# Performance work log

Measured on AMD Instinct MI355X. Metric: run time of the kernel, lower is better.

Reference implementation:

```python
import jax, jax.numpy as jnp
import numpy as np

B, N, K, H, NF = 4, 4096, 20, 64, 128
EPS = 1e-5  # BatchNorm eps (inference mode)


def _knn_idx(x):
    # x: (B, C, N); returns indices of K nearest neighbors (incl. self), (B, N, K)
    xx = jnp.sum(x * x, axis=1)                      # (B, N)
    inner = jnp.einsum('bcn,bcm->bnm', x, x)         # (B, N, N)
    neg_dist = 2.0 * inner - xx[:, :, None] - xx[:, None, :]
    return jax.lax.top_k(neg_dist, K)[1]


def _graph_feat(x, first):
    # x: (B, C, N) -> edge features (B, C', N, K)
    idx = _knn_idx(x)                                # (B, N, K)
    xt = jnp.transpose(x, (0, 2, 1))                 # (B, N, C)
    nb = jax.vmap(lambda f, i: f[i])(xt, idx)        # (B, N, K, C)
    nb = jnp.transpose(nb, (0, 3, 1, 2))             # (B, C, N, K)
    c = jnp.broadcast_to(x[:, :, :, None], nb.shape)
    parts = [nb - c]
    if first:  # cross term only in first block (3-dim coords)
        parts.append(jnp.cross(c, nb, axis=1))
    parts.append(c)
    return jnp.concatenate(parts, axis=1)


def _conv_bn_lrelu(x, W, g, b, m, v):
    # 1x1 conv (no bias) + BatchNorm (inference) + LeakyReLU(0.2)
    y = jnp.einsum('oc,bc...->bo...', W, x)
    scale = g / jnp.sqrt(v + EPS)
    sh = (1, -1) + (1,) * (y.ndim - 2)
    y = y * scale.reshape(sh) + (b - m * scale).reshape(sh)
    return jnp.where(y >= 0, y, 0.2 * y)


def _forward(x, layers, We, Wh, bh):
    x = jnp.transpose(x, (0, 2, 1))                  # (B, 3, N)
    outs = []
    for li in range(4):
        gf = _graph_feat(x, li == 0)                 # (B, cin, N, K)
        y = _conv_bn_lrelu(gf, *layers[li])          # (B, cout, N, K)
        x = jnp.max(y, axis=-1)                      # max-pool over neighbors
        outs.append(x)
    cat = jnp.concatenate(outs, axis=1)              # (B, 512, N)
    y = _conv_bn_lrelu(cat, *layers[4])              # final Conv1d block
    y = jnp.max(y, axis=-1)                          # global max over points
    emb = y @ We.T                                   # Linear(512, NF, bias=False)
    return emb @ Wh.T + bh                           # embedding_head


def setup_inputs() -> dict:
    key = jax.random.key(0)
    ks = jax.random.split(key, 40)

    def nrm(k, shape, s=0.1):
        return jax.random.normal(k, shape, jnp.float32) * s

    inp = {'x': jax.random.normal(ks[0], (B, N, 3), jnp.float32)}
    dims = [(9, H), (2 * H, H), (2 * H, 2 * H), (4 * H, 4 * H), (8 * H, 8 * H)]
    i = 1
    for li, (cin, cout) in enumerate(dims):
        inp['W%d' % li] = nrm(ks[i], (cout, cin)); i += 1
        inp['g%d' % li] = 1.0 + nrm(ks[i], (cout,), 0.05); i += 1
        inp['b%d' % li] = nrm(ks[i], (cout,), 0.05); i += 1
        inp['m%d' % li] = nrm(ks[i], (cout,), 0.05); i += 1
        inp['v%d' % li] = 1.0 + jax.random.uniform(ks[i], (cout,)) * 0.1; i += 1
    inp['We'] = nrm(ks[i], (NF, 8 * H)); i += 1
    inp['Wh'] = nrm(ks[i], (NF, NF)); i += 1
    inp['bh'] = nrm(ks[i], (NF,))
    return inp


def reference(x, W0, g0, b0, m0, v0, W1, g1, b1, m1, v1, W2, g2, b2, m2, v2,
              W3, g3, b3, m3, v3, W4, g4, b4, m4, v4, We, Wh, bh):
    layers = [(W0, g0, b0, m0, v0), (W1, g1, b1, m1, v1), (W2, g2, b2, m2, v2),
              (W3, g3, b3, m3, v3), (W4, g4, b4, m4, v4)]
    return _forward(x, layers, We, Wh, bh)
```

## Files before the change

### kernel.cpp

```cpp
#include <hip/hip_runtime.h>
#include <cfloat>

#define N_PTS 4096
#define NB    4
#define KNN   20
#define EPSB  1e-5f
#define NSL   4

typedef short s8v __attribute__((ext_vector_type(8)));
typedef float f4v __attribute__((ext_vector_type(4)));

__device__ __forceinline__ void bf16split(float x, unsigned short* h, unsigned short* l)
{
    unsigned u = __builtin_bit_cast(unsigned, x);
    unsigned hb = (u + 0x7fffu + ((u >> 16) & 1u)) >> 16;
    float hf = __builtin_bit_cast(float, hb << 16);
    float res = x - hf;
    unsigned u2 = __builtin_bit_cast(unsigned, res);
    unsigned lb = (u2 + 0x7fffu + ((u2 >> 16) & 1u)) >> 16;
    *h = (unsigned short)hb;
    *l = (unsigned short)lb;
}

__device__ __forceinline__ unsigned packkey(float d, int lc)
{
    d = fmaxf(d, 0.f);
    unsigned u = __builtin_bit_cast(unsigned, d);
    return (u & 0xFFFFFF00u) | (unsigned)lc;
}

__device__ __forceinline__ void insert20k(unsigned key, unsigned (&k20)[KNN])
{
#pragma unroll
    for (int j = 0; j < KNN; j++) {
        unsigned old = k20[j];
        unsigned lo = old < key ? old : key;
        key = old < key ? key : old;
        k20[j] = lo;
    }
}

__device__ __forceinline__ void gl2lds16(const void* g, void* l)
{
    __builtin_amdgcn_global_load_lds(
        (const __attribute__((address_space(1))) unsigned int*)g,
        (__attribute__((address_space(3))) unsigned int*)l,
        16, 0, 0);
}

__device__ __forceinline__ int swz(int g)
{
    return g ^ (((g >> 3) ^ (g >> 6)) & 7);
}

__global__ __launch_bounds__(256)
void to_bf16_pm(const float* __restrict__ F, long bsF, int ldF, int C, int KDP,
                unsigned short* __restrict__ Ghi, unsigned short* __restrict__ Glo)
{
    int b = blockIdx.y;
    int n = blockIdx.x * 64 + (threadIdx.x & 63);
    int kq = threadIdx.x >> 6;
    const float* Fr = F + (long)b * bsF + (long)n * ldF;
    for (int k0 = kq * 8; k0 < KDP; k0 += 32) {
        s8v hv, lv;
#pragma unroll
        for (int i = 0; i < 8; i++) {
            int k = k0 + i;
            float x = (k < C) ? Fr[k] : 0.f;
            unsigned short h, l;
            bf16split(x, &h, &l);
            hv[i] = (short)h;
            lv[i] = (short)l;
        }
        long o = ((long)b * N_PTS + n) * KDP + k0;
        *(s8v*)&Ghi[o] = hv;
        *(s8v*)&Glo[o] = lv;
    }
}

__global__ void sqnorm_pm(const float* __restrict__ F, float* __restrict__ xx,
                          int C, int ldF, long bsF)
{
    int b = blockIdx.y;
    int i = blockIdx.x * 256 + threadIdx.x;
    const float* r = F + (long)b * bsF + (long)i * ldF;
    float s = 0.f;
    for (int c = 0; c < C; c++) s = fmaf(r[c], r[c], s);
    xx[(long)b * N_PTS + i] = s;
}

template<int KDP>
__global__ __launch_bounds__(256, 3)
void fused_knn_mfma7(const unsigned short* __restrict__ Ghi,
                     const unsigned short* __restrict__ Glo,
                     const float* __restrict__ xx,
                     float* __restrict__ knnd, int* __restrict__ knni)
{
    constexpr int KS = KDP / 32;
    constexpr int TS = 16 * KDP;
    constexpr int NCH = (TS * 2) / 16;
    __shared__ short cbuf[2][2][TS];
    __shared__ unsigned mk[4][16][4][KNN];

    int tid = threadIdx.x;
    int w = tid >> 6, L = tid & 63;
    int n = L & 15;
    int quad = L >> 4;
    int b = blockIdx.z, slice = blockIdx.y;
    int q0 = blockIdx.x * 64, qw = w * 16;
    const unsigned short* Gh = Ghi + (long)b * N_PTS * KDP;
    const unsigned short* Gl = Glo + (long)b * N_PTS * KDP;
    const float* xxb = xx + (long)b * N_PTS;

    s8v qhi[KS], qlo[KS];
    long qbase = (long)(q0 + qw + n) * KDP + quad * 8;
#pragma unroll
    for (int ks = 0; ks < KS; ks++) {
        qhi[ks] = *(const s8v*)&Gh[qbase + ks * 32];
        qlo[ks] = *(const s8v*)&Gl[qbase + ks * 32];
    }
    float xq = xxb[q0 + qw + n];

    unsigned k20[KNN];
#pragma unroll
    for (int j = 0; j < KNN; j++) k20[j] = 0xFFFFFFFFu;

    int po[KS];
#pragma unroll
    for (int ks = 0; ks < KS; ks++) {
        int gL = n * (KDP / 8) + quad + ks * 4;
        po[ks] = swz(gL) * 8;
    }
    int gsrc = swz(tid);

    int w64 = tid & 192;
    {
        long tb = (long)(slice * 1024) * KDP;
        if (tid < NCH) {
            gl2lds16((const char*)(Gh + tb) + gsrc * 16,
                     (char*)&cbuf[0][0][0] + w64 * 16);
            gl2lds16((const char*)(Gl + tb) + gsrc * 16,
                     (char*)&cbuf[0][1][0] + w64 * 16);
        }
    }
    __syncthreads();

    const float* xcp = xxb + slice * 1024 + quad * 4;

    for (int t = 0; t < 64; t++) {
        int cur = t & 1;
        if (t < 63 && tid < NCH) {
            long tb = (long)(slice * 1024 + (t + 1) * 16) * KDP;
            gl2lds16((const char*)(Gh + tb) + gsrc * 16,
                     (char*)&cbuf[cur ^ 1][0][0] + w64 * 16);
            gl2lds16((const char*)(Gl + tb) + gsrc * 16,
                     (char*)&cbuf[cur ^ 1][1][0] + w64 * 16);
        }

        const short* Ch = &cbuf[cur][0][0];
        const short* Cl = &cbuf[cur][1][0];
        f4v acc = {0.f, 0.f, 0.f, 0.f};
#pragma unroll
        for (int ks = 0; ks < KS; ks++) {
            s8v chi = *(const s8v*)&Ch[po[ks]];
            s8v clo = *(const s8v*)&Cl[po[ks]];
            acc = __builtin_amdgcn_mfma_f32_16x16x32_bf16(chi, qhi[ks], acc, 0, 0, 0);
            acc = __builtin_amdgcn_mfma_f32_16x16x32_bf16(chi, qlo[ks], acc, 0, 0, 0);
            acc = __builtin_amdgcn_mfma_f32_16x16x32_bf16(clo, qhi[ks], acc, 0, 0, 0);
        }
        float4 xc4 = *(const float4*)xcp;
        float xcv[4] = {xc4.x, xc4.y, xc4.z, xc4.w};
#pragma unroll
        for (int r = 0; r < 4; r++) {
            float d = xq + xcv[r] - 2.f * acc[r];
            insert20k(packkey(d, t * 4 + r), k20);
        }
        xcp += 16;
        __syncthreads();
    }

#pragma unroll
    for (int j = 0; j < KNN; j++) mk[w][n][quad][j] = k20[j];
    __syncthreads();
    if (L < 16) {
        int p[4] = {0, 0, 0, 0};
        long o = (((long)b * NSL + slice) * N_PTS + (q0 + qw + L)) * KNN;
#pragma unroll
        for (int j = 0; j < KNN; j++) {
            unsigned bd = 0xFFFFFF00u; int bi = 0x7fffffff; int bq = 0;
#pragma unroll
            for (int qd = 0; qd < 4; qd++) {
                unsigned kk = mk[w][L][qd][p[qd]];
                unsigned db = kk & 0xFFFFFF00u;
                int lc = (int)(kk & 0xFFu);
                int ci = slice * 1024 + (lc >> 2) * 16 + qd * 4 + (lc & 3);
                if (db < bd || (db == bd && ci < bi)) { bd = db; bi = ci; bq = qd; }
            }
            knnd[o + j] = __builtin_bit_cast(float, bd);
            knni[o + j] = bi;
            p[bq]++;
        }
    }
}

__global__ void knn_merge4(const float* __restrict__ knnd, const int* __restrict__ knni,
                           int* __restrict__ idxOut)
{
    int id = blockIdx.x * 256 + threadIdx.x;
    int b = id / N_PTS, i = id % N_PTS;
    const float* dl[NSL]; const int* il[NSL];
#pragma unroll
    for (int qt = 0; qt < NSL; qt++) {
        dl[qt] = knnd + (((long)b * NSL + qt) * N_PTS + i) * KNN;
        il[qt] = knni + (((long)b * NSL + qt) * N_PTS + i) * KNN;
    }
    int p[NSL];
#pragma unroll
    for (int qt = 0; qt < NSL; qt++) p[qt] = 0;
    int* o = idxOut + (long)id * KNN;
#pragma unroll
    for (int j = 0; j < KNN; j++) {
        float best = FLT_MAX; int bi = 0x7fffffff; int bq = 0;
#pragma unroll
        for (int qt = 0; qt < NSL; qt++) {
            float vv = (p[qt] < KNN) ? dl[qt][p[qt]] : FLT_MAX;
            int   ci = (p[qt] < KNN) ? il[qt][p[qt]] : 0x7fffffff;
            if (vv < best || (vv == best && ci < bi)) { best = vv; bi = ci; bq = qt; }
        }
        o[j] = bi;
        p[bq]++;
    }
}

template<int KDP>
__global__ __launch_bounds__(256)
void qp_mfma(const unsigned short* __restrict__ Ghi,
             const unsigned short* __restrict__ Glo,
             const unsigned short* __restrict__ Wqh, const unsigned short* __restrict__ Wql,
             const unsigned short* __restrict__ Wph, const unsigned short* __restrict__ Wpl,
             const float* __restrict__ shf,
             float* __restrict__ qv, float* __restrict__ pv, int cout)
{
    constexpr int KS = KDP / 32;
    int tid = threadIdx.x;
    int w = tid >> 6, L = tid & 63;
    int n = L & 15, quad = L >> 4;
    int b = blockIdx.z;
    int p0 = blockIdx.x * 64 + w * 16;

    s8v ah[KS], al[KS];
    long abase = ((long)b * N_PTS + p0 + n) * KDP + quad * 8;
#pragma unroll
    for (int ks = 0; ks < KS; ks++) {
        ah[ks] = *(const s8v*)&Ghi[abase + ks * 32];
        al[ks] = *(const s8v*)&Glo[abase + ks * 32];
    }

#pragma unroll
    for (int oc4 = 0; oc4 < 4; oc4++) {
        int oc = blockIdx.y * 4 + oc4;
        long wbase = (long)(oc * 16 + n) * KDP + quad * 8;
        f4v aq = {0.f, 0.f, 0.f, 0.f};
        f4v ap = {0.f, 0.f, 0.f, 0.f};
#pragma unroll
        for (int ks = 0; ks < KS; ks++) {
            s8v wh = *(const s8v*)&Wqh[wbase + ks * 32];
            s8v wl = *(const s8v*)&Wql[wbase + ks * 32];
            aq = __builtin_amdgcn_mfma_f32_16x16x32_bf16(ah[ks], wh, aq, 0, 0, 0);
            aq = __builtin_amdgcn_mfma_f32_16x16x32_bf16(ah[ks], wl, aq, 0, 0, 0);
            aq = __builtin_amdgcn_mfma_f32_16x16x32_bf16(al[ks], wh, aq, 0, 0, 0);
            s8v ph = *(const s8v*)&Wph[wbase + ks * 32];
            s8v pl = *(const s8v*)&Wpl[wbase + ks * 32];
            ap = __builtin_amdgcn_mfma_f32_16x16x32_bf16(ah[ks], ph, ap, 0, 0, 0);
            ap = __builtin_amdgcn_mfma_f32_16x16x32_bf16(ah[ks], pl, ap, 0, 0, 0);
            ap = __builtin_amdgcn_mfma_f32_16x16x32_bf16(al[ks], ph, ap, 0, 0, 0);
        }
        float sv = shf[oc * 16 + n];
#pragma unroll
        for (int r = 0; r < 4; r++) {
            long pt = p0 + quad * 4 + r;
            long o = ((long)b * N_PTS + pt) * cout + oc * 16 + n;
            qv[o] = aq[r];
            pv[o] = ap[r] + sv;
        }
    }
}

__global__ __launch_bounds__(256)
void conv4g_mfma(const float* __restrict__ cat,
                 const unsigned short* __restrict__ W4h, const unsigned short* __restrict__ W4l,
                 const float* __restrict__ shf, float* __restrict__ Y)
{
    int tid = threadIdx.x;
    int w = tid >> 6, L = tid & 63;
    int n = L & 15, quad = L >> 4;
    int b = blockIdx.z;
    int p0 = blockIdx.x * 64 + w * 16;
    int ob0 = blockIdx.y * 64;

    const float* cr = cat + ((long)b * N_PTS + p0 + n) * 512 + quad * 8;

    f4v acc[4];
#pragma unroll
    for (int c4 = 0; c4 < 4; c4++) acc[c4] = {0.f, 0.f, 0.f, 0.f};

    for (int ks = 0; ks < 16; ks++) {
        float4 f0 = *(const float4*)&cr[ks * 32];
        float4 f1 = *(const float4*)&cr[ks * 32 + 4];
        float fv[8] = {f0.x, f0.y, f0.z, f0.w, f1.x, f1.y, f1.z, f1.w};
        s8v ah, al;
#pragma unroll
        for (int i = 0; i < 8; i++) {
            unsigned short h, l;
            bf16split(fv[i], &h, &l);
            ah[i] = (short)h;
            al[i] = (short)l;
        }
#pragma unroll
        for (int c4 = 0; c4 < 4; c4++) {
            long wb = (long)(ob0 + c4 * 16 + n) * 512 + quad * 8 + ks * 32;
            s8v wh = *(const s8v*)&W4h[wb];
            s8v wl = *(const s8v*)&W4l[wb];
            acc[c4] = __builtin_amdgcn_mfma_f32_16x16x32_bf16(ah, wh, acc[c4], 0, 0, 0);
            acc[c4] = __builtin_amdgcn_mfma_f32_16x16x32_bf16(ah, wl, acc[c4], 0, 0, 0);
            acc[c4] = __builtin_amdgcn_mfma_f32_16x16x32_bf16(al, wh, acc[c4], 0, 0, 0);
        }
    }
#pragma unroll
    for (int c4 = 0; c4 < 4; c4++) {
        int o = ob0 + c4 * 16 + n;
        float sv = shf[o];
#pragma unroll
        for (int r = 0; r < 4; r++) {
            int pt = p0 + quad * 4 + r;
            float y = acc[c4][r] + sv;
            y = y >= 0.f ? y : 0.2f * y;
            Y[((long)b * 512 + o) * N_PTS + pt] = y;
        }
    }
}

__global__ void fold_edge_bf16(const float* __restrict__ W, const float* __restrict__ g,
                               const float* __restrict__ bb, const float* __restrict__ m,
                               const float* __restrict__ v,
                               unsigned short* __restrict__ Wqh, unsigned short* __restrict__ Wql,
                               unsigned short* __restrict__ Wph, unsigned short* __restrict__ Wpl,
                               float* __restrict__ shift, int C, int cout)
{
    int id = blockIdx.x * 256 + threadIdx.x;
    if (id < C * cout) {
        int o = id / C;
        int c = id % C;
        float sc = g[o] * rsqrtf(v[o] + EPSB);
        float wd = W[(long)o * 2 * C + c];
        float wc = W[(long)o * 2 * C + C + c];
        bf16split(sc * wd, &Wqh[id], &Wql[id]);
        bf16split(sc * (wc - wd), &Wph[id], &Wpl[id]);
    }
    if (id < cout) {
        float sc = g[id] * rsqrtf(v[id] + EPSB);
        shift[id] = bb[id] - m[id] * sc;
    }
}

__global__ void fold_plain_bf16(const float* __restrict__ W, const float* __restrict__ g,
                                const float* __restrict__ bb, const float* __restrict__ m,
                                const float* __restrict__ v,
                                unsigned short* __restrict__ W4h, unsigned short* __restrict__ W4l,
                                float* __restrict__ shift, int C, int cout)
{
    int id = blockIdx.x * 256 + threadIdx.x;
    if (id < C * cout) {
        int o = id / C;
        int c = id % C;
        float sc = g[o] * rsqrtf(v[o] + EPSB);
        bf16split(sc * W[(long)o * C + c], &W4h[id], &W4l[id]);
    }
    if (id < cout) {
        float sc = g[id] * rsqrtf(v[id] + EPSB);
        shift[id] = bb[id] - m[id] * sc;
    }
}

__global__ void gather_max_fused(const float* __restrict__ q, const float* __restrict__ p,
                                 const int* __restrict__ idx, float* __restrict__ cat,
                                 int cout, int c_off,
                                 unsigned short* __restrict__ Ghi,
                                 unsigned short* __restrict__ Glo,
                                 float* __restrict__ xx)
{
    int b = blockIdx.y;
    int i = blockIdx.x * 4 + threadIdx.y;
    int tx = threadIdx.x;
    const int* ip = idx + ((long)b * N_PTS + i) * KNN;
    int js[KNN];
#pragma unroll
    for (int k = 0; k < KNN; k++) js[k] = ip[k];
    const float* qb = q + (long)b * N_PTS * cout;
    const float* pb = p + ((long)b * N_PTS + i) * cout;
    float* ob = cat + ((long)b * N_PTS + i) * 512 + c_off;
    float ssum = 0.f;
    for (int o0 = 0; o0 < cout; o0 += 64) {
        int o = o0 + tx;
        float pv = pb[o];
        float mx = -FLT_MAX;
#pragma unroll
        for (int k = 0; k < KNN; k++) {
            float val = qb[(long)js[k] * cout + o] + pv;
            val = val >= 0.f ? val : 0.2f * val;
            mx = fmaxf(mx, val);
        }
        ob[o] = mx;
        if (Ghi) {
            unsigned short h, l;
            bf16split(mx, &h, &l);
            long go = ((long)b * N_PTS + i) * cout + o;
            Ghi[go] = h;
            Glo[go] = l;
            ssum = fmaf(mx, mx, ssum);
        }
    }
    if (Ghi) {
#pragma unroll
        for (int off = 32; off > 0; off >>= 1) ssum += __shfl_xor(ssum, off);
        if (tx == 0) xx[(long)b * N_PTS + i] = ssum;
    }
}

__global__ void edge0_fused(const float* __restrict__ x, const int* __restrict__ idx,
                            const float* __restrict__ W0, const float* __restrict__ g0,
                            const float* __restrict__ b0, const float* __restrict__ m0,
                            const float* __restrict__ v0, float* __restrict__ cat,
                            unsigned short* __restrict__ Ghi,
                            unsigned short* __restrict__ Glo,
                            float* __restrict__ xx)
{
    int b = blockIdx.y;
    int i = blockIdx.x * 4 + threadIdx.y;
    int o = threadIdx.x;
    const float* xc = x + ((long)b * N_PTS + i) * 3;
    float cx = xc[0], cy = xc[1], cz = xc[2];
    float w[9];
#pragma unroll
    for (int c = 0; c < 9; c++) w[c] = W0[o * 9 + c];
    float sc = g0[o] * rsqrtf(v0[o] + EPSB);
    float sh = b0[o] - m0[o] * sc;
    const int* ip = idx + ((long)b * N_PTS + i) * KNN;
    float mx = -FLT_MAX;
#pragma unroll
    for (int k = 0; k < KNN; k++) {
        const float* xn = x + ((long)b * N_PTS + ip[k]) * 3;
        float nx = xn[0], ny = xn[1], nz = xn[2];
        float dx = nx - cx, dy = ny - cy, dz = nz - cz;
        float crx = cy * nz - cz * ny;
        float cry = cz * nx - cx * nz;
        float crz = cx * ny - cy * nx;
        float y = w[0] * dx + w[1] * dy + w[2] * dz
                + w[3] * crx + w[4] * cry + w[5] * crz
                + w[6] * cx + w[7] * cy + w[8] * cz;
        y = y * sc + sh;
        y = y >= 0.f ? y : 0.2f * y;
        mx = fmaxf(mx, y);
    }
    cat[((long)b * N_PTS + i) * 512 + o] = mx;
    unsigned short h, l;
    bf16split(mx, &h, &l);
    long go = ((long)b * N_PTS + i) * 64 + o;
    Ghi[go] = h;
    Glo[go] = l;
    float ssum = mx * mx;
#pragma unroll
    for (int off = 32; off > 0; off >>= 1) ssum += __shfl_xor(ssum, off);
    if (o == 0) xx[(long)b * N_PTS + i] = ssum;
}

__global__ void rowmax_kernel(const float* __restrict__ Y, float* __restrict__ ymax)
{
    __shared__ float red[256];
    int b = blockIdx.y, o = blockIdx.x, t = threadIdx.x;
    const float* yb = Y + ((long)b * 512 + o) * N_PTS;
    float mx = -FLT_MAX;
#pragma unroll
    for (int s = 0; s < N_PTS / 256; s++) mx = fmaxf(mx, yb[t + 256 * s]);
    red[t] = mx;
    __syncthreads();
    for (int off = 128; off > 0; off >>= 1) {
        if (t < off) red[t] = fmaxf(red[t], red[t + off]);
        __syncthreads();
    }
    if (t == 0) ymax[(long)b * 512 + o] = red[0];
}

__global__ void head_kernel(const float* __restrict__ ymax, const float* __restrict__ We,
                            const float* __restrict__ Wh, const float* __restrict__ bh,
                            float* __restrict__ out)
{
    __shared__ float emb[128];
    __shared__ float yv[512];
    int b = blockIdx.x, t = threadIdx.x;
    for (int s = t; s < 512; s += 128) yv[s] = ymax[(long)b * 512 + s];
    __syncthreads();
    float acc = 0.f;
    for (int c = 0; c < 512; c++) acc = fmaf(yv[c], We[(long)t * 512 + c], acc);
    emb[t] = acc;
    __syncthreads();
    float acc2 = bh[t];
    for (int ff = 0; ff < 128; ff++) acc2 = fmaf(emb[ff], Wh[(long)t * 128 + ff], acc2);
    out[(long)b * 128 + t] = acc2;
}

extern "C" void kernel_launch(void* const* d_in, const int* in_sizes, int n_in,
                              void* d_out, int out_size, void* d_ws, size_t ws_size,
                              hipStream_t stream)
{
    const float* x = (const float*)d_in[0];
    const float *W[5], *g[5], *bb[5], *m[5], *v[5];
    for (int li = 0; li < 5; li++) {
        W[li]  = (const float*)d_in[1 + li * 5 + 0];
        g[li]  = (const float*)d_in[1 + li * 5 + 1];
        bb[li] = (const float*)d_in[1 + li * 5 + 2];
        m[li]  = (const float*)d_in[1 + li * 5 + 3];
        v[li]  = (const float*)d_in[1 + li * 5 + 4];
    }
    const float* We = (const float*)d_in[26];
    const float* Wh = (const float*)d_in[27];
    const float* bh = (const float*)d_in[28];
    float* out = (float*)d_out;

    float* ws   = (float*)d_ws;
    float* cat  = ws;
    float* qbuf = cat + (long)8388608;
    float* pbuf = qbuf + (long)8388608;
    int*   idxb = (int*)(pbuf + 4194304);
    float* xx   = (float*)(idxb + 327680);
    unsigned short* Wqh = (unsigned short*)(xx + 16384);
    unsigned short* Wql = Wqh + 32768;
    unsigned short* Wph = Wql + 32768;
    unsigned short* Wpl = Wph + 32768;
    unsigned short* W4h = Wpl + 32768;
    unsigned short* W4l = W4h + 262144;
    float* shf  = (float*)(W4l + 262144);
    float* ymax = shf + 512;
    unsigned short* Ghi = (unsigned short*)qbuf;
    unsigned short* Glo = Ghi + 2097152;
    float* knnd = qbuf + 2097152;
    int*   knni = (int*)(qbuf + 2097152 + 1310720);
    float* qv   = qbuf + 2097152;
    float* Ybuf = qbuf;

    sqnorm_pm<<<dim3(16, NB), dim3(256), 0, stream>>>(x, xx, 3, 3, (long)3 * N_PTS);
    to_bf16_pm<<<dim3(64, NB), dim3(256), 0, stream>>>(
        x, (long)3 * N_PTS, 3, 3, 32, Ghi, Glo);
    fused_knn_mfma7<32><<<dim3(64, NSL, NB), dim3(256), 0, stream>>>(
        Ghi, Glo, xx, knnd, knni);
    knn_merge4<<<dim3(64), dim3(256), 0, stream>>>(knnd, knni, idxb);
    edge0_fused<<<dim3(N_PTS / 4, NB), dim3(64, 4), 0, stream>>>(
        x, idxb, W[0], g[0], bb[0], m[0], v[0], cat, Ghi, Glo, xx);

    const int Cs_[3]   = {64, 64, 128};
    const int co_[3]   = {64, 128, 256};
    const int outO_[3] = {64, 128, 256};
    for (int s = 0; s < 3; s++) {
        int C = Cs_[s], cout = co_[s];
        if (C == 64)
            fused_knn_mfma7<64><<<dim3(64, NSL, NB), dim3(256), 0, stream>>>(
                Ghi, Glo, xx, knnd, knni);
        else
            fused_knn_mfma7<128><<<dim3(64, NSL, NB), dim3(256), 0, stream>>>(
                Ghi, Glo, xx, knnd, knni);
        knn_merge4<<<dim3(64), dim3(256), 0, stream>>>(knnd, knni, idxb);

        int li = s + 1;
        fold_edge_bf16<<<dim3((C * cout + 255) / 256), dim3(256), 0, stream>>>(
            W[li], g[li], bb[li], m[li], v[li], Wqh, Wql, Wph, Wpl, shf, C, cout);
        if (C == 64)
            qp_mfma<64><<<dim3(64, cout / 64, NB), dim3(256), 0, stream>>>(
                Ghi, Glo, Wqh, Wql, Wph, Wpl, shf, qv, pbuf, cout);
        else
            qp_mfma<128><<<dim3(64, cout / 64, NB), dim3(256), 0, stream>>>(
                Ghi, Glo, Wqh, Wql, Wph, Wpl, shf, qv, pbuf, cout);
        if (s < 2)
            gather_max_fused<<<dim3(N_PTS / 4, NB), dim3(64, 4), 0, stream>>>(
                qv, pbuf, idxb, cat, cout, outO_[s], Ghi, Glo, xx);
        else
            gather_max_fused<<<dim3(N_PTS / 4, NB), dim3(64, 4), 0, stream>>>(
                qv, pbuf, idxb, cat, cout, outO_[s],
                (unsigned short*)nullptr, (unsigned short*)nullptr, (float*)nullptr);
    }

    fold_plain_bf16<<<dim3((512 * 512 + 255) / 256), dim3(256), 0, stream>>>(
        W[4], g[4], bb[4], m[4], v[4], W4h, W4l, shf, 512, 512);
    conv4g_mfma<<<dim3(N_PTS / 64, 8, NB), dim3(256), 0, stream>>>(
        cat, W4h, W4l, shf, Ybuf);

    rowmax_kernel<<<dim3(512, NB), dim3(256), 0, stream>>>(Ybuf, ymax);
    head_kernel<<<dim3(NB), dim3(128), 0, stream>>>(ymax, We, Wh, bh, out);
}
```

Measured before the change: 1.084 ms.

## Double-buffer conv4 weight and activation tiles in LDS via async global-to-LDS loads

The final 512x512 conv kernel now stages each K-slice of the split bf16 weights and the fp32 input tile into shared memory with direct global-to-LDS loads. It double-buffers them so the next slice's loads overlap the current slice's MFMAs. Before this, every wave read weights and inputs straight from global memory. The change adds one block barrier per K step and relies on existing swizzle and gl2lds16 helpers defined elsewhere in the file.

```diff
diff --git a/kernel.cpp b/kernel.cpp
--- a/kernel.cpp
+++ b/kernel.cpp
@@ -287,27 +287,66 @@
 }
 
 __global__ __launch_bounds__(256)
-void conv4g_mfma(const float* __restrict__ cat,
+void conv4h_mfma(const float* __restrict__ cat,
                  const unsigned short* __restrict__ W4h, const unsigned short* __restrict__ W4l,
                  const float* __restrict__ shf, float* __restrict__ Y)
 {
+    __shared__ short Wbs[2][2][2048];
+    __shared__ float Cbs[2][2048];
+
     int tid = threadIdx.x;
     int w = tid >> 6, L = tid & 63;
     int n = L & 15, quad = L >> 4;
     int b = blockIdx.z;
-    int p0 = blockIdx.x * 64 + w * 16;
+    int p0b = blockIdx.x * 64;
     int ob0 = blockIdx.y * 64;
-
-    const float* cr = cat + ((long)b * N_PTS + p0 + n) * 512 + quad * 8;
+    int w64 = tid & 192;
+
+    const char* catb = (const char*)(cat + ((long)b * N_PTS + p0b) * 512);
+    const char* whb  = (const char*)(W4h + (long)ob0 * 512);
+    const char* wlb  = (const char*)(W4l + (long)ob0 * 512);
+
+    int gw = swz(tid);
+    int gc0 = swz(tid);
+    int gc1 = swz(tid + 256);
+
+    long woff = (long)(gw >> 2) * 1024 + (gw & 3) * 16;
+    long coff0 = (long)(gc0 >> 3) * 2048 + (gc0 & 7) * 16;
+    long coff1 = (long)(gc1 >> 3) * 2048 + (gc1 & 7) * 16;
+
+    {
+        gl2lds16(whb + woff, (char*)&Wbs[0][0][0] + w64 * 16);
+        gl2lds16(wlb + woff, (char*)&Wbs[0][1][0] + w64 * 16);
+        gl2lds16(catb + coff0, (char*)&Cbs[0][0] + w64 * 16);
+        gl2lds16(catb + coff1, (char*)&Cbs[0][0] + (256 + w64) * 16);
+    }
+    __syncthreads();
+
+    int p8 = (w * 16 + n) * 8;
+    int cch0 = swz(p8 + quad * 2) * 16;
+    int cch1 = swz(p8 + quad * 2 + 1) * 16;
+    int wch[4];
+#pragma unroll
+    for (int c4 = 0; c4 < 4; c4++) wch[c4] = swz((c4 * 16 + n) * 4 + quad) * 16;
 
     f4v acc[4];
 #pragma unroll
     for (int c4 = 0; c4 < 4; c4++) acc[c4] = {0.f, 0.f, 0.f, 0.f};
 
     for (int ks = 0; ks < 16; ks++) {
-        float4 f0 = *(const float4*)&cr[ks * 32];
-        float4 f1 = *(const float4*)&cr[ks * 32 + 4];
-        float fv[8] = {f0.x, f0.y, f0.z, f0.w, f1.x, f1.y, f1.z, f1.w};
+        int cur = ks & 1;
+        if (ks < 15) {
+            long t2 = (long)(ks + 1) * 64;
+            long tc = (long)(ks + 1) * 128;
+            gl2lds16(whb + t2 + woff, (char*)&Wbs[cur ^ 1][0][0] + w64 * 16);
+            gl2lds16(wlb + t2 + woff, (char*)&Wbs[cur ^ 1][1][0] + w64 * 16);
+            gl2lds16(catb + tc + coff0, (char*)&Cbs[cur ^ 1][0] + w64 * 16);
+            gl2lds16(catb + tc + coff1, (char*)&Cbs[cur ^ 1][0] + (256 + w64) * 16);
+        }
+
+        float4 c0 = *(const float4*)((const char*)&Cbs[cur][0] + cch0);
+        float4 c1 = *(const float4*)((const char*)&Cbs[cur][0] + cch1);
+        float fv[8] = {c0.x, c0.y, c0.z, c0.w, c1.x, c1.y, c1.z, c1.w};
         s8v ah, al;
 #pragma unroll
         for (int i = 0; i < 8; i++) {
@@ -318,21 +357,22 @@
         }
 #pragma unroll
         for (int c4 = 0; c4 < 4; c4++) {
-            long wb = (long)(ob0 + c4 * 16 + n) * 512 + quad * 8 + ks * 32;
-            s8v wh = *(const s8v*)&W4h[wb];
-            s8v wl = *(const s8v*)&W4l[wb];
+            s8v wh = *(const s8v*)((const char*)&Wbs[cur][0][0] + wch[c4]);
+            s8v wl = *(const s8v*)((const char*)&Wbs[cur][1][0] + wch[c4]);
             acc[c4] = __builtin_amdgcn_mfma_f32_16x16x32_bf16(ah, wh, acc[c4], 0, 0, 0);
             acc[c4] = __builtin_amdgcn_mfma_f32_16x16x32_bf16(ah, wl, acc[c4], 0, 0, 0);
             acc[c4] = __builtin_amdgcn_mfma_f32_16x16x32_bf16(al, wh, acc[c4], 0, 0, 0);
         }
-    }
+        __syncthreads();
+    }
+
 #pragma unroll
     for (int c4 = 0; c4 < 4; c4++) {
         int o = ob0 + c4 * 16 + n;
         float sv = shf[o];
 #pragma unroll
         for (int r = 0; r < 4; r++) {
-            int pt = p0 + quad * 4 + r;
+            int pt = p0b + w * 16 + quad * 4 + r;
             float y = acc[c4][r] + sv;
             y = y >= 0.f ? y : 0.2f * y;
             Y[((long)b * 512 + o) * N_PTS + pt] = y;
@@ -590,7 +630,7 @@
 
     fold_plain_bf16<<<dim3((512 * 512 + 255) / 256), dim3(256), 0, stream>>>(
         W[4], g[4], bb[4], m[4], v[4], W4h, W4l, shf, 512, 512);
-    conv4g_mfma<<<dim3(N_PTS / 64, 8, NB), dim3(256), 0, stream>>>(
+    conv4h_mfma<<<dim3(N_PTS / 64, 8, NB), dim3(256), 0, stream>>>(
         cat, W4h, W4l, shf, Ybuf);
 
     rowmax_kernel<<<dim3(512, NB), dim3(256), 0, stream>>>(Ybuf, ymax);
```

After: 943.9 us, median of 2. -13.0%, faster.
